# Kernel optimization log

Hardware: AMD Instinct MI355X
Metric: run time of the kernel (lower is better)

Reference implementation:

```python
import jax, jax.numpy as jnp
import numpy as np

N_SRC, N_DST, E, D, H = 100000, 10000, 320000, 128, 128
LN_EPS = 1e-5


def setup_inputs() -> dict:
    key = jax.random.key(0)
    ks = jax.random.split(key, 12)
    h_src = jax.random.normal(ks[0], (N_SRC, D), jnp.float32)
    h_dst = jax.random.normal(ks[1], (N_DST, D), jnp.float32)
    s_emb = jax.random.normal(ks[2], (N_DST, D), jnp.float32)
    edge_weight = jax.random.uniform(ks[3], (E,), jnp.float32)
    src_idx = jax.random.randint(ks[4], (E,), 0, N_SRC)
    dst_idx = jnp.sort(jax.random.randint(ks[5], (E,), 0, N_DST))
    # session_attention: Linear(2D->H, no bias) -> tanh -> Linear(H->1, no bias)
    W1 = jax.random.normal(ks[6], (2 * D, H), jnp.float32) / np.sqrt(2 * D)
    w2 = jax.random.normal(ks[7], (H,), jnp.float32) / np.sqrt(H)
    # output_proj: Linear(2D->D) with bias
    Wo = jax.random.normal(ks[8], (2 * D, D), jnp.float32) / np.sqrt(2 * D)
    bo = jnp.zeros((D,), jnp.float32)
    gamma = jnp.ones((D,), jnp.float32)
    beta = jnp.zeros((D,), jnp.float32)
    return {"h_src": h_src, "h_dst": h_dst, "s_emb": s_emb,
            "edge_weight": edge_weight, "src_idx": src_idx, "dst_idx": dst_idx,
            "W1": W1, "w2": w2, "Wo": Wo, "bo": bo, "gamma": gamma, "beta": beta}


def reference(h_src, h_dst, s_emb, edge_weight, src_idx, dst_idx, W1, w2, Wo, bo, gamma, beta):
    d = h_src.shape[1]
    # concat([h_src[src], s_emb[dst]]) @ W1 == h_src[src] @ W1[:d] + s_emb[dst] @ W1[d:]
    # project per-node first (cheaper than per-edge concat matmul)
    p_src = h_src @ W1[:d]          # [N_src, H]
    p_dst = s_emb @ W1[d:]          # [N_dst, H]
    raw = jnp.tanh(p_src[src_idx] + p_dst[dst_idx]) @ w2   # [E]
    raw = raw * edge_weight
    # edge_softmax: segment softmax over incoming edges of each dst node
    seg_max = jax.ops.segment_max(raw, dst_idx, num_segments=h_dst.shape[0])
    seg_max = jnp.where(jnp.isfinite(seg_max), seg_max, 0.0)  # handle degree-0 dsts
    ex = jnp.exp(raw - seg_max[dst_idx])
    den = jax.ops.segment_sum(ex, dst_idx, num_segments=h_dst.shape[0])
    attn = ex / den[dst_idx]                                 # [E]
    # u_mul_e + sum: weighted gather-scatter aggregation
    h_global = jax.ops.segment_sum(h_src[src_idx] * attn[:, None], dst_idx,
                                   num_segments=h_dst.shape[0])  # [N_dst, D]
    # output_proj on concat([h_dst, h_global])
    out = h_dst @ Wo[:d] + h_global @ Wo[d:] + bo
    # residual + layer norm (dropout = identity in eval)
    x = h_dst + out
    mu = jnp.mean(x, axis=-1, keepdims=True)
    var = jnp.mean((x - mu) ** 2, axis=-1, keepdims=True)
    y = (x - mu) / jnp.sqrt(var + LN_EPS) * gamma + beta
    return (y, attn[:, None])
```

## Files before the change

kernel.cpp:

```cpp
#include <hip/hip_runtime.h>
#include <math.h>

#define D128 128
#define SCAPW 256

typedef unsigned int uint32;
typedef unsigned short ushort_t;
typedef short bf16x8 __attribute__((ext_vector_type(8)));
typedef float f32x4 __attribute__((ext_vector_type(4)));
typedef float f32x2 __attribute__((ext_vector_type(2)));

__device__ __forceinline__ ushort_t bf16_of(float x) {
  uint32 u = __float_as_uint(x);
  return (ushort_t)((u + 0x7fffu + ((u >> 16) & 1u)) >> 16);
}
__device__ __forceinline__ uint32 pack_bf2(float x, float y) {
  uint32 bx = __float_as_uint(x);
  uint32 by = __float_as_uint(y);
  bx = (bx + 0x7fffu + ((bx >> 16) & 1u)) >> 16;
  by = (by + 0x7fffu + ((by >> 16) & 1u)) & 0xffff0000u;
  return bx | by;
}
__device__ __forceinline__ float bf_lo(uint32 u) { return __uint_as_float(u << 16); }
__device__ __forceinline__ float bf_hi(uint32 u) { return __uint_as_float(u & 0xffff0000u); }

__device__ __forceinline__ float fast_tanh(float x) {
  float e = __expf(2.0f * x);
  float r = __builtin_amdgcn_rcpf(1.0f + e);
  return fmaf(-2.0f, r, 1.0f);
}

__device__ __forceinline__ uint32 pack_fp8x4(float a, float b, float c, float d) {
  int u = __builtin_amdgcn_cvt_pk_fp8_f32(a, b, 0, false);
  u = __builtin_amdgcn_cvt_pk_fp8_f32(c, d, u, true);
  return (uint32)u;
}

__global__ __launch_bounds__(256) void prep_all(
    const float* __restrict__ h_src, const float* __restrict__ s_emb,
    const float* __restrict__ h_dst,
    const float* __restrict__ W1, const float* __restrict__ Wo,
    const int* __restrict__ dst_idx,
    uint32* __restrict__ h_src_bf, uint32* __restrict__ s_emb_bf,
    uint32* __restrict__ h_dst_bf, uint32* __restrict__ h_src_f8,
    ushort_t* __restrict__ Wfrag, ushort_t* __restrict__ Wo_frag,
    int* __restrict__ off,
    int n_src_el, int n_dst_el, int E, int N, int nb_conv) {
  const int b = blockIdx.x;
  const int tid = threadIdx.x;
  if (b < nb_conv) {
    int i = (b * 256 + tid) * 8;
    const int n_bf_el = n_src_el + 2 * n_dst_el;
    if (i < n_bf_el) {
      const float* src;
      uint32* dst;
      if (i < n_src_el) { src = h_src + i; dst = h_src_bf + (i >> 1); }
      else if (i < n_src_el + n_dst_el) {
        src = s_emb + (i - n_src_el); dst = s_emb_bf + ((i - n_src_el) >> 1);
      } else {
        src = h_dst + (i - n_src_el - n_dst_el);
        dst = h_dst_bf + ((i - n_src_el - n_dst_el) >> 1);
      }
      float4 a = *(const float4*)src;
      float4 c = *(const float4*)(src + 4);
      uint4 p;
      p.x = pack_bf2(a.x, a.y);
      p.y = pack_bf2(a.z, a.w);
      p.z = pack_bf2(c.x, c.y);
      p.w = pack_bf2(c.z, c.w);
      *(uint4*)dst = p;
    } else {
      int k = i - n_bf_el;
      if (k >= n_src_el) return;
      float4 a = *(const float4*)(h_src + k);
      float4 c = *(const float4*)(h_src + k + 4);
      uint2 p;
      p.x = pack_fp8x4(a.x, a.y, a.z, a.w);
      p.y = pack_fp8x4(c.x, c.y, c.z, c.w);
      *(uint2*)(h_src_f8 + (k >> 2)) = p;
    }
  } else if (b < nb_conv + 16) {
    int t = (b - nb_conv) * 256 + tid;
    int lane = t & 63;
    int kc = (t >> 6) & 3;
    int nt = (t >> 8) & 7;
    int h = (t >> 11) & 1;
    int m = lane & 15;
    int quad = lane >> 4;
    int krow = h * D128 + kc * 32 + quad * 8;
    int ncol = nt * 16 + m;
    ushort_t fr[8];
#pragma unroll
    for (int j = 0; j < 8; j++) fr[j] = bf16_of(W1[(size_t)(krow + j) * D128 + ncol]);
    *(uint4*)(Wfrag + (size_t)t * 8) = *(const uint4*)fr;
  } else if (b < nb_conv + 32) {
    int t = (b - nb_conv - 16) * 256 + tid;
    int lane = t & 63;
    int kc = (t >> 6) & 7;
    int nt = (t >> 9) & 7;
    int m = lane & 15;
    int quad = lane >> 4;
    int krow = kc * 32 + quad * 8;
    int ncol = nt * 16 + m;
    ushort_t fr[8];
#pragma unroll
    for (int j = 0; j < 8; j++) fr[j] = bf16_of(Wo[(size_t)(krow + j) * D128 + ncol]);
    *(uint4*)(Wo_frag + (size_t)t * 8) = *(const uint4*)fr;
  } else {
    int e = (b - nb_conv - 32) * 256 + tid;
    if (e >= E) return;
    int d = dst_idx[e];
    int dprev = (e == 0) ? -1 : dst_idx[e - 1];
    for (int v = dprev + 1; v <= d; v++) off[v] = e;
    if (e == E - 1) {
      for (int v = d + 1; v <= N; v++) off[v] = E;
    }
  }
}

__global__ __launch_bounds__(256) void gemm_mfma(
    const ushort_t* __restrict__ Xa, const ushort_t* __restrict__ Xb,
    const ushort_t* __restrict__ Wfrag,
    uint32* __restrict__ Pa, uint32* __restrict__ Pb,
    int Ma, int Mb, int nblk_a) {
  __shared__ uint32 Ys8[128][36];
  const int blk = blockIdx.x;
  const ushort_t* X;
  const bf16x8* Wf;
  uint32* P;
  int M, row0;
  if (blk < nblk_a) { X = Xa; P = Pa; Wf = (const bf16x8*)Wfrag;           M = Ma; row0 = blk * 128; }
  else              { X = Xb; P = Pb; Wf = (const bf16x8*)(Wfrag + 16384); M = Mb; row0 = (blk - nblk_a) * 128; }

  const int tid = threadIdx.x;
  const int wave = tid >> 6;
  const int lane = tid & 63;
  const int m = lane & 15;
  const int quad = lane >> 4;

  const int ra0 = min(row0 + wave * 32 + m, M - 1);
  const int ra1 = min(row0 + wave * 32 + 16 + m, M - 1);

  f32x4 acc[2][8];
#pragma unroll
  for (int st = 0; st < 2; st++)
#pragma unroll
    for (int nt = 0; nt < 8; nt++) acc[st][nt] = (f32x4){0.f, 0.f, 0.f, 0.f};

#pragma unroll
  for (int kc = 0; kc < 4; kc++) {
    bf16x8 x0 = *(const bf16x8*)(X + (size_t)ra0 * D128 + kc * 32 + quad * 8);
    bf16x8 x1 = *(const bf16x8*)(X + (size_t)ra1 * D128 + kc * 32 + quad * 8);
#pragma unroll
    for (int nt = 0; nt < 8; nt++) {
      bf16x8 wf = Wf[(nt * 4 + kc) * 64 + lane];
      acc[0][nt] = __builtin_amdgcn_mfma_f32_16x16x32_bf16(wf, x0, acc[0][nt], 0, 0, 0);
      acc[1][nt] = __builtin_amdgcn_mfma_f32_16x16x32_bf16(wf, x1, acc[1][nt], 0, 0, 0);
    }
  }

#pragma unroll
  for (int st = 0; st < 2; st++)
#pragma unroll
    for (int nt = 0; nt < 8; nt++)
      Ys8[wave * 32 + st * 16 + m][nt * 4 + quad] =
          pack_fp8x4(acc[st][nt][0], acc[st][nt][1], acc[st][nt][2], acc[st][nt][3]);
  __syncthreads();

#pragma unroll
  for (int it = 0; it < 4; it++) {
    int f = tid + 256 * it;
    int row = f >> 3;
    int cu = (f & 7) * 4;
    int grow = row0 + row;
    if (grow < M) *(uint4*)(P + (size_t)grow * 32 + cu) = *(const uint4*)(&Ys8[row][cu]);
  }
}

__global__ __launch_bounds__(256) void attn_agg_kernel(
    const uint32* __restrict__ p_src_f8, const uint32* __restrict__ p_dst_f8,
    const float* __restrict__ w2, const float* __restrict__ ew,
    const int* __restrict__ src_idx, const int* __restrict__ off,
    const uint32* __restrict__ h_src_f8,
    float* __restrict__ attn_out, uint32* __restrict__ h_glob_bf, int N_dst) {
  const int tid = threadIdx.x;
  const int wv = tid >> 6;
  const int lane = tid & 63;
  const int v = blockIdx.x * 4 + wv;

  __shared__ float sex[4][SCAPW];
  if (v >= N_dst) return;

  const int lo = off[v], hi = off[v + 1];
  const int deg = hi - lo;
  const int sub = lane & 15;
  const int eg = lane >> 4;
  const bool fast = (deg <= SCAPW);

  float4 wA = *(const float4*)(w2 + sub * 8);
  float4 wB = *(const float4*)(w2 + sub * 8 + 4);
  uint2 pdu = *(const uint2*)(p_dst_f8 + (size_t)v * 32 + sub * 2);
  f32x2 pd0 = __builtin_amdgcn_cvt_pk_f32_fp8(pdu.x, false);
  f32x2 pd1 = __builtin_amdgcn_cvt_pk_f32_fp8(pdu.x, true);
  f32x2 pd2 = __builtin_amdgcn_cvt_pk_f32_fp8(pdu.y, false);
  f32x2 pd3 = __builtin_amdgcn_cvt_pk_f32_fp8(pdu.y, true);

  float den = 0.f;
  float acc[8];
#pragma unroll
  for (int j = 0; j < 8; j++) acc[j] = 0.f;

  for (int base = 0; base < deg; base += 4) {
    const int ei = base + eg;
    float ex = 0.f;
    if (ei < deg) {
      const int e = lo + ei;
      const int s = src_idx[e];
      const float ewv = ew[e];
      uint2 us = *(const uint2*)(p_src_f8 + (size_t)s * 32 + sub * 2);
      f32x2 a0 = __builtin_amdgcn_cvt_pk_f32_fp8(us.x, false);
      f32x2 a1 = __builtin_amdgcn_cvt_pk_f32_fp8(us.x, true);
      f32x2 a2 = __builtin_amdgcn_cvt_pk_f32_fp8(us.y, false);
      f32x2 a3 = __builtin_amdgcn_cvt_pk_f32_fp8(us.y, true);
      float sc;
      sc = fast_tanh(a0.x + pd0.x) * wA.x;
      sc = fmaf(fast_tanh(a0.y + pd0.y), wA.y, sc);
      sc = fmaf(fast_tanh(a1.x + pd1.x), wA.z, sc);
      sc = fmaf(fast_tanh(a1.y + pd1.y), wA.w, sc);
      sc = fmaf(fast_tanh(a2.x + pd2.x), wB.x, sc);
      sc = fmaf(fast_tanh(a2.y + pd2.y), wB.y, sc);
      sc = fmaf(fast_tanh(a3.x + pd3.x), wB.z, sc);
      sc = fmaf(fast_tanh(a3.y + pd3.y), wB.w, sc);
#pragma unroll
      for (int o = 1; o <= 8; o <<= 1) sc += __shfl_xor(sc, o, 64);
      ex = __expf(sc * ewv);
      if (sub == 0) {
        if (fast) sex[wv][ei] = ex;
        else attn_out[lo + ei] = ex;
      }
      uint2 uh = *(const uint2*)(h_src_f8 + (size_t)s * 32 + sub * 2);
      f32x2 h0 = __builtin_amdgcn_cvt_pk_f32_fp8(uh.x, false);
      f32x2 h1 = __builtin_amdgcn_cvt_pk_f32_fp8(uh.x, true);
      f32x2 h2 = __builtin_amdgcn_cvt_pk_f32_fp8(uh.y, false);
      f32x2 h3 = __builtin_amdgcn_cvt_pk_f32_fp8(uh.y, true);
      acc[0] = fmaf(ex, h0.x, acc[0]);
      acc[1] = fmaf(ex, h0.y, acc[1]);
      acc[2] = fmaf(ex, h1.x, acc[2]);
      acc[3] = fmaf(ex, h1.y, acc[3]);
      acc[4] = fmaf(ex, h2.x, acc[4]);
      acc[5] = fmaf(ex, h2.y, acc[5]);
      acc[6] = fmaf(ex, h3.x, acc[6]);
      acc[7] = fmaf(ex, h3.y, acc[7]);
    }
    den += (sub == 0) ? ex : 0.f;
  }

#pragma unroll
  for (int o = 1; o <= 32; o <<= 1) den += __shfl_xor(den, o, 64);
  const float inv = (deg > 0) ? 1.0f / den : 0.0f;

  if (fast) {
    for (int i = lane; i < deg; i += 64) attn_out[lo + i] = sex[wv][i] * inv;
  } else {
    for (int i = lane; i < deg; i += 64) attn_out[lo + i] *= inv;
  }

#pragma unroll
  for (int j = 0; j < 8; j++) {
    acc[j] += __shfl_xor(acc[j], 16, 64);
    acc[j] += __shfl_xor(acc[j], 32, 64);
  }
  if (eg == 0) {
    uint4 o;
    o.x = pack_bf2(acc[0] * inv, acc[1] * inv);
    o.y = pack_bf2(acc[2] * inv, acc[3] * inv);
    o.z = pack_bf2(acc[4] * inv, acc[5] * inv);
    o.w = pack_bf2(acc[6] * inv, acc[7] * inv);
    *(uint4*)(h_glob_bf + (size_t)v * 64 + sub * 4) = o;
  }
}

__global__ __launch_bounds__(128) void out_mfma_ln(
    const ushort_t* __restrict__ h_dst_bf, const ushort_t* __restrict__ h_glob_bf,
    const ushort_t* __restrict__ Wo_frag,
    const float* __restrict__ h_dst, const float* __restrict__ bo,
    const float* __restrict__ gamma, const float* __restrict__ beta,
    float* __restrict__ y, int N) {
  __shared__ float sbo[128], sgam[128], sbet[128];
  const int tid = threadIdx.x;
  if (tid < 128) { sbo[tid] = bo[tid]; sgam[tid] = gamma[tid]; sbet[tid] = beta[tid]; }
  __syncthreads();

  const int w = tid >> 6;
  const int lane = tid & 63;
  const int m = lane & 15;
  const int quad = lane >> 4;
  const int row0 = blockIdx.x * 32 + w * 16;
  const int ra = min(row0 + m, N - 1);
  const bf16x8* Wf = (const bf16x8*)Wo_frag;

  f32x4 acc[8];
#pragma unroll
  for (int nt = 0; nt < 8; nt++) acc[nt] = (f32x4){0.f, 0.f, 0.f, 0.f};

#pragma unroll
  for (int kc = 0; kc < 8; kc++) {
    const ushort_t* X = (kc < 4) ? h_dst_bf : h_glob_bf;
    const int kk = kc & 3;
    bf16x8 a = *(const bf16x8*)(X + (size_t)ra * D128 + kk * 32 + quad * 8);
#pragma unroll
    for (int nt = 0; nt < 8; nt++) {
      bf16x8 bfr = Wf[(nt * 8 + kc) * 64 + lane];
      acc[nt] = __builtin_amdgcn_mfma_f32_16x16x32_bf16(a, bfr, acc[nt], 0, 0, 0);
    }
  }

#pragma unroll
  for (int r = 0; r < 4; r++) {
    const int grow = row0 + quad * 4 + r;
    const int gr = min(grow, N - 1);
    float x[8];
    float s1 = 0.f, s2 = 0.f;
#pragma unroll
    for (int nt = 0; nt < 8; nt++) {
      float hd = h_dst[(size_t)gr * D128 + nt * 16 + m];
      float xv = hd + acc[nt][r] + sbo[nt * 16 + m];
      x[nt] = xv;
      s1 += xv;
      s2 = fmaf(xv, xv, s2);
    }
#pragma unroll
    for (int o = 1; o <= 8; o <<= 1) {
      s1 += __shfl_xor(s1, o, 64);
      s2 += __shfl_xor(s2, o, 64);
    }
    float mu = s1 * (1.0f / 128.0f);
    float var = s2 * (1.0f / 128.0f) - mu * mu;
    float rstd = __builtin_amdgcn_rcpf(sqrtf(var + 1e-5f));
    if (grow < N) {
#pragma unroll
      for (int nt = 0; nt < 8; nt++) {
        int c = nt * 16 + m;
        y[(size_t)grow * D128 + c] = (x[nt] - mu) * rstd * sgam[c] + sbet[c];
      }
    }
  }
}

extern "C" void kernel_launch(void* const* d_in, const int* in_sizes, int n_in,
                              void* d_out, int out_size, void* d_ws, size_t ws_size,
                              hipStream_t stream) {
  const float* h_src = (const float*)d_in[0];
  const float* h_dst = (const float*)d_in[1];
  const float* s_emb = (const float*)d_in[2];
  const float* ew    = (const float*)d_in[3];
  const int* src_idx = (const int*)d_in[4];
  const int* dst_idx = (const int*)d_in[5];
  const float* W1    = (const float*)d_in[6];
  const float* w2    = (const float*)d_in[7];
  const float* Wo    = (const float*)d_in[8];
  const float* bo    = (const float*)d_in[9];
  const float* gamma = (const float*)d_in[10];
  const float* beta  = (const float*)d_in[11];

  const int N_src = in_sizes[0] / D128;
  const int N_dst = in_sizes[1] / D128;
  const int E = in_sizes[3];

  float* out_y = (float*)d_out;
  float* out_attn = out_y + (size_t)N_dst * D128;

  uint32* p_src_f8 = (uint32*)d_ws;
  uint32* p_dst_f8 = p_src_f8 + (size_t)N_src * 32;
  uint32* h_src_f8 = p_dst_f8 + (size_t)N_dst * 32;
  uint32* h_src_bf = h_src_f8 + (size_t)N_src * 32;
  uint32* h_dst_bf = h_src_bf + (size_t)N_src * 64;
  uint32* h_glob_bf = h_dst_bf + (size_t)N_dst * 64;
  uint32* s_emb_bf = h_glob_bf + (size_t)N_dst * 64;
  int* seg_off = (int*)(s_emb_bf + (size_t)N_dst * 64);
  ushort_t* Wfrag = (ushort_t*)(seg_off + N_dst + 1 + 3);
  ushort_t* Wo_frag = Wfrag + 32768;

  const int n_src_el = N_src * D128;
  const int n_dst_el = N_dst * D128;
  const int n_conv_el = 2 * n_src_el + 2 * n_dst_el;
  const int nblk_a = (N_src + 127) / 128;
  const int nblk_b = (N_dst + 127) / 128;
  const int nb_conv = (n_conv_el / 8 + 255) / 256;
  const int nb_seg = (E + 255) / 256;

  prep_all<<<nb_conv + 32 + nb_seg, 256, 0, stream>>>(
      h_src, s_emb, h_dst, W1, Wo, dst_idx,
      h_src_bf, s_emb_bf, h_dst_bf, h_src_f8, Wfrag, Wo_frag, seg_off,
      n_src_el, n_dst_el, E, N_dst, nb_conv);
  gemm_mfma<<<nblk_a + nblk_b, 256, 0, stream>>>(
      (const ushort_t*)h_src_bf, (const ushort_t*)s_emb_bf, Wfrag,
      p_src_f8, p_dst_f8, N_src, N_dst, nblk_a);
  attn_agg_kernel<<<(N_dst + 3) / 4, 256, 0, stream>>>(
      p_src_f8, p_dst_f8, w2, ew, src_idx, seg_off, h_src_f8, out_attn,
      h_glob_bf, N_dst);
  out_mfma_ln<<<(N_dst + 31) / 32, 128, 0, stream>>>(
      (const ushort_t*)h_dst_bf, (const ushort_t*)h_glob_bf, Wo_frag,
      h_dst, bo, gamma, beta, out_y, N_dst);
}
```

Measured before the change: 181.8 us.

## Fuse bf16/fp8 h_src conversion and split aggregation into separate LDS-driven pass

The prep kernel now reads h_src once and writes both the bf16 and fp8 copies in the same thread. This removes a second full read of h_src and shrinks the conversion grid. The attention kernel stores each edge's softmax numerator and source index in LDS during the score loop, then runs a second pass where 32 lanes each gather one 4-byte fp8 word per row, processing two edges per wavefront step. This replaces the 16-lane, four-edge gather and its cross-group reduction. The trade-off is extra LDS traffic and a second loop over the edges, plus reloading src_idx and attn_out for high-degree nodes.

```diff
diff --git a/kernel.cpp b/kernel.cpp
--- a/kernel.cpp
+++ b/kernel.cpp
@@ -50,12 +50,23 @@
   const int tid = threadIdx.x;
   if (b < nb_conv) {
     int i = (b * 256 + tid) * 8;
-    const int n_bf_el = n_src_el + 2 * n_dst_el;
-    if (i < n_bf_el) {
+    if (i < n_src_el) {
+      float4 a = *(const float4*)(h_src + i);
+      float4 c = *(const float4*)(h_src + i + 4);
+      uint4 p;
+      p.x = pack_bf2(a.x, a.y);
+      p.y = pack_bf2(a.z, a.w);
+      p.z = pack_bf2(c.x, c.y);
+      p.w = pack_bf2(c.z, c.w);
+      *(uint4*)(h_src_bf + (i >> 1)) = p;
+      uint2 q;
+      q.x = pack_fp8x4(a.x, a.y, a.z, a.w);
+      q.y = pack_fp8x4(c.x, c.y, c.z, c.w);
+      *(uint2*)(h_src_f8 + (i >> 2)) = q;
+    } else if (i < n_src_el + 2 * n_dst_el) {
       const float* src;
       uint32* dst;
-      if (i < n_src_el) { src = h_src + i; dst = h_src_bf + (i >> 1); }
-      else if (i < n_src_el + n_dst_el) {
+      if (i < n_src_el + n_dst_el) {
         src = s_emb + (i - n_src_el); dst = s_emb_bf + ((i - n_src_el) >> 1);
       } else {
         src = h_dst + (i - n_src_el - n_dst_el);
@@ -69,15 +80,6 @@
       p.z = pack_bf2(c.x, c.y);
       p.w = pack_bf2(c.z, c.w);
       *(uint4*)dst = p;
-    } else {
-      int k = i - n_bf_el;
-      if (k >= n_src_el) return;
-      float4 a = *(const float4*)(h_src + k);
-      float4 c = *(const float4*)(h_src + k + 4);
-      uint2 p;
-      p.x = pack_fp8x4(a.x, a.y, a.z, a.w);
-      p.y = pack_fp8x4(c.x, c.y, c.z, c.w);
-      *(uint2*)(h_src_f8 + (k >> 2)) = p;
     }
   } else if (b < nb_conv + 16) {
     int t = (b - nb_conv) * 256 + tid;
@@ -189,6 +191,7 @@
   const int v = blockIdx.x * 4 + wv;
 
   __shared__ float sex[4][SCAPW];
+  __shared__ int ssrc[4][SCAPW];
   if (v >= N_dst) return;
 
   const int lo = off[v], hi = off[v + 1];
@@ -206,10 +209,6 @@
   f32x2 pd3 = __builtin_amdgcn_cvt_pk_f32_fp8(pdu.y, true);
 
   float den = 0.f;
-  float acc[8];
-#pragma unroll
-  for (int j = 0; j < 8; j++) acc[j] = 0.f;
-
   for (int base = 0; base < deg; base += 4) {
     const int ei = base + eg;
     float ex = 0.f;
@@ -235,48 +234,68 @@
       for (int o = 1; o <= 8; o <<= 1) sc += __shfl_xor(sc, o, 64);
       ex = __expf(sc * ewv);
       if (sub == 0) {
-        if (fast) sex[wv][ei] = ex;
+        if (fast) { sex[wv][ei] = ex; ssrc[wv][ei] = s; }
         else attn_out[lo + ei] = ex;
       }
-      uint2 uh = *(const uint2*)(h_src_f8 + (size_t)s * 32 + sub * 2);
-      f32x2 h0 = __builtin_amdgcn_cvt_pk_f32_fp8(uh.x, false);
-      f32x2 h1 = __builtin_amdgcn_cvt_pk_f32_fp8(uh.x, true);
-      f32x2 h2 = __builtin_amdgcn_cvt_pk_f32_fp8(uh.y, false);
-      f32x2 h3 = __builtin_amdgcn_cvt_pk_f32_fp8(uh.y, true);
-      acc[0] = fmaf(ex, h0.x, acc[0]);
-      acc[1] = fmaf(ex, h0.y, acc[1]);
-      acc[2] = fmaf(ex, h1.x, acc[2]);
-      acc[3] = fmaf(ex, h1.y, acc[3]);
-      acc[4] = fmaf(ex, h2.x, acc[4]);
-      acc[5] = fmaf(ex, h2.y, acc[5]);
-      acc[6] = fmaf(ex, h3.x, acc[6]);
-      acc[7] = fmaf(ex, h3.y, acc[7]);
     }
     den += (sub == 0) ? ex : 0.f;
   }
-
 #pragma unroll
   for (int o = 1; o <= 32; o <<= 1) den += __shfl_xor(den, o, 64);
   const float inv = (deg > 0) ? 1.0f / den : 0.0f;
 
+  const int c4 = lane & 31;
+  const int hw = lane >> 5;
+  float a0 = 0.f, a1 = 0.f, a2 = 0.f, a3 = 0.f;
+
   if (fast) {
+    const int pad = (deg + 15) & ~15;
+    for (int i = deg + lane; i < pad; i += 64) { sex[wv][i] = 0.f; ssrc[wv][i] = 0; }
     for (int i = lane; i < deg; i += 64) attn_out[lo + i] = sex[wv][i] * inv;
+    for (int b = 0; b < pad; b += 16) {
+#pragma unroll
+      for (int j = 0; j < 8; j++) {
+        const int idx = b + j * 2 + hw;
+        float ex = sex[wv][idx];
+        int s = ssrc[wv][idx];
+        uint32 u = h_src_f8[(size_t)s * 32 + c4];
+        f32x2 h0 = __builtin_amdgcn_cvt_pk_f32_fp8(u, false);
+        f32x2 h1 = __builtin_amdgcn_cvt_pk_f32_fp8(u, true);
+        a0 = fmaf(ex, h0.x, a0);
+        a1 = fmaf(ex, h0.y, a1);
+        a2 = fmaf(ex, h1.x, a2);
+        a3 = fmaf(ex, h1.y, a3);
+      }
+    }
   } else {
+    for (int b = 0; b < deg; b += 16) {
+#pragma unroll
+      for (int j = 0; j < 8; j++) {
+        const int idx = b + j * 2 + hw;
+        float ex = 0.f;
+        int s = 0;
+        if (idx < deg) { ex = attn_out[lo + idx]; s = src_idx[lo + idx]; }
+        uint32 u = h_src_f8[(size_t)s * 32 + c4];
+        f32x2 h0 = __builtin_amdgcn_cvt_pk_f32_fp8(u, false);
+        f32x2 h1 = __builtin_amdgcn_cvt_pk_f32_fp8(u, true);
+        a0 = fmaf(ex, h0.x, a0);
+        a1 = fmaf(ex, h0.y, a1);
+        a2 = fmaf(ex, h1.x, a2);
+        a3 = fmaf(ex, h1.y, a3);
+      }
+    }
     for (int i = lane; i < deg; i += 64) attn_out[lo + i] *= inv;
   }
 
-#pragma unroll
-  for (int j = 0; j < 8; j++) {
-    acc[j] += __shfl_xor(acc[j], 16, 64);
-    acc[j] += __shfl_xor(acc[j], 32, 64);
-  }
-  if (eg == 0) {
-    uint4 o;
-    o.x = pack_bf2(acc[0] * inv, acc[1] * inv);
-    o.y = pack_bf2(acc[2] * inv, acc[3] * inv);
-    o.z = pack_bf2(acc[4] * inv, acc[5] * inv);
-    o.w = pack_bf2(acc[6] * inv, acc[7] * inv);
-    *(uint4*)(h_glob_bf + (size_t)v * 64 + sub * 4) = o;
+  a0 += __shfl_xor(a0, 32, 64);
+  a1 += __shfl_xor(a1, 32, 64);
+  a2 += __shfl_xor(a2, 32, 64);
+  a3 += __shfl_xor(a3, 32, 64);
+  if (hw == 0) {
+    uint2 o;
+    o.x = pack_bf2(a0 * inv, a1 * inv);
+    o.y = pack_bf2(a2 * inv, a3 * inv);
+    *(uint2*)(h_glob_bf + (size_t)v * 64 + c4 * 2) = o;
   }
 }
 
@@ -383,7 +402,7 @@
 
   const int n_src_el = N_src * D128;
   const int n_dst_el = N_dst * D128;
-  const int n_conv_el = 2 * n_src_el + 2 * n_dst_el;
+  const int n_conv_el = n_src_el + 2 * n_dst_el;
   const int nblk_a = (N_src + 127) / 128;
   const int nblk_b = (N_dst + 127) / 128;
   const int nb_conv = (n_conv_el / 8 + 255) / 256;
```

After: 173.7 us. 1.05x faster.
